# Performance work log

Hardware: AMD Instinct MI355X
Metric: run time of the kernel (lower is better)

## Reference

```python
import jax, jax.numpy as jnp
import numpy as np

HEADS = 4
DIM_HEAD = 32
EPS = 1e-5

def _layernorm(x, g, b):
    mu = jnp.mean(x, axis=-1, keepdims=True)
    var = jnp.var(x, axis=-1, keepdims=True)
    return (x - mu) * jax.lax.rsqrt(var + EPS) * g + b

def setup_inputs() -> dict:
    key = jax.random.key(0)
    ks = jax.random.split(key, 8)
    B, C, H, W = 16, 256, 32, 32
    N = H * W
    inner = HEADS * DIM_HEAD  # 128
    s = lambda d: 1.0 / np.sqrt(d)
    return {
        "x": jax.random.normal(ks[0], (B, C, H, W), jnp.float32),
        "pos_embedding": jax.random.normal(ks[1], (1, N, C), jnp.float32),
        "w_qkv": jax.random.normal(ks[2], (C, inner * 3), jnp.float32) * s(C),
        "w_out": jax.random.normal(ks[3], (inner, C), jnp.float32) * s(inner),
        "b_out": jnp.zeros((C,), jnp.float32),
        "w_ff1": jax.random.normal(ks[4], (C, inner), jnp.float32) * s(C),
        "b_ff1": jnp.zeros((inner,), jnp.float32),
        "w_ff2": jax.random.normal(ks[5], (inner, C), jnp.float32) * s(inner),
        "b_ff2": jnp.zeros((C,), jnp.float32),
        "g1": jnp.ones((C,), jnp.float32),
        "beta1": jnp.zeros((C,), jnp.float32),
        "g2": jnp.ones((C,), jnp.float32),
        "beta2": jnp.zeros((C,), jnp.float32),
    }

def reference(x, pos_embedding, w_qkv, w_out, b_out, w_ff1, b_ff1, w_ff2, b_ff2, g1, beta1, g2, beta2):
    b, c, h, w = x.shape
    n = h * w
    tok = jnp.transpose(x.reshape(b, c, n), (0, 2, 1))  # [b, n, c]
    tok = tok + pos_embedding  # (dropout is identity at eval)
    # attention
    qkv = _layernorm(tok, g1, beta1) @ w_qkv  # [b, n, 3*inner]
    qkv = qkv.reshape(b, n, 3, HEADS, DIM_HEAD)
    q, k, v = qkv[:, :, 0], qkv[:, :, 1], qkv[:, :, 2]  # [b, n, h, d]
    scale = DIM_HEAD ** -0.5
    dots = jnp.einsum('bihd,bjhd->bhij', q, k) * scale
    attn = jax.nn.softmax(dots, axis=-1)
    out = jnp.einsum('bhij,bjhd->bihd', attn, v).reshape(b, n, HEADS * DIM_HEAD)
    tok = out @ w_out + b_out + tok
    # ffn
    hdn = jax.nn.gelu(_layernorm(tok, g2, beta2) @ w_ff1 + b_ff1, approximate=False)
    tok = hdn @ w_ff2 + b_ff2 + tok
    return jnp.transpose(tok, (0, 2, 1)).reshape(b, c, h, w)
```

## Files before the change

### kernel.cpp

```cpp
#include <hip/hip_runtime.h>
#include <hip/hip_bf16.h>
#include <math.h>

#define B_     16
#define C_     256
#define N_     1024
#define HEADS_ 4
#define DH_    32
#define INNER_ 128
#define EPS_   1e-5f

typedef __attribute__((ext_vector_type(8))) short bf16x8;
typedef __attribute__((ext_vector_type(4))) float f32x4;

__device__ __forceinline__ ushort f2bf(float f) {
  union { float f; unsigned u; } v; v.f = f;
  unsigned u = v.u;
  return (ushort)((u + 0x7fffu + ((u >> 16) & 1u)) >> 16);
}
__device__ __forceinline__ float bf2f(ushort u) {
  union { unsigned u; float f; } v; v.u = ((unsigned)u) << 16;
  return v.f;
}
__device__ __forceinline__ unsigned cvt_pk_bf16(float lo, float hi) {
  unsigned r;
  asm("v_cvt_pk_bf16_f32 %0, %1, %2" : "=v"(r) : "v"(lo), "v"(hi));
  return r;
}

#define QSCALE_ 0.2550348652979437f

__global__ __launch_bounds__(256) void k_wconv(
    const float* __restrict__ wqkv, const float* __restrict__ wout,
    const float* __restrict__ wff1, const float* __restrict__ wff2,
    ushort* __restrict__ wqkvT, ushort* __restrict__ woutT,
    ushort* __restrict__ wff1T, ushort* __restrict__ wff2T) {
  int i = blockIdx.x * 256 + threadIdx.x;
  if (i < 98304) {
    int k = i / 384, n = i % 384;
    wqkvT[n * 256 + k] = f2bf(wqkv[i]);
    return;
  }
  i -= 98304;
  if (i < 32768) {
    int k = i / 256, n = i % 256;
    woutT[n * 128 + k] = f2bf(wout[i]);
    return;
  }
  i -= 32768;
  if (i < 32768) {
    int k = i / 128, n = i % 128;
    wff1T[n * 256 + k] = f2bf(wff1[i]);
    return;
  }
  i -= 32768;
  {
    int k = i / 256, n = i % 256;
    wff2T[n * 128 + k] = f2bf(wff2[i]);
  }
}

union KFusedSmem {
  float  xs[C_][68];
  ushort xnl[64][264];
};

__global__ __launch_bounds__(512) void k_fused(
    const float* __restrict__ x, const float* __restrict__ pos,
    const float* __restrict__ g1, const float* __restrict__ beta1,
    const ushort* __restrict__ wqkvT, ushort* __restrict__ tokb,
    ushort* __restrict__ qb, ushort* __restrict__ kb, ushort* __restrict__ vtb) {
  const int b  = blockIdx.x >> 4;
  const int n0 = (blockIdx.x & 15) << 6;
  const int t  = threadIdx.x;
  __shared__ KFusedSmem u;

  {
    const int nq = t & 15, cq = t >> 4;
#pragma unroll
    for (int i = 0; i < 8; ++i) {
      const int c = i * 32 + cq;
      const float4 v = *reinterpret_cast<const float4*>(
          &x[((size_t)b * C_ + c) * N_ + n0 + 4 * nq]);
      *reinterpret_cast<float4*>(&u.xs[c][4 * nq]) = v;
    }
  }
  __syncthreads();

  {
    const int tl = t >> 3, sub = t & 7, c0 = sub * 32;
    const int n = n0 + tl;
    float v[32];
#pragma unroll
    for (int i = 0; i < 32; ++i) v[i] = u.xs[c0 + i][tl];
#pragma unroll
    for (int j = 0; j < 8; ++j) {
      const float4 p = *reinterpret_cast<const float4*>(&pos[(size_t)n * C_ + c0 + 4 * j]);
      v[4*j] += p.x; v[4*j+1] += p.y; v[4*j+2] += p.z; v[4*j+3] += p.w;
    }
    float s = 0.f;
#pragma unroll
    for (int i = 0; i < 32; ++i) s += v[i];
    s += __shfl_xor(s, 1); s += __shfl_xor(s, 2); s += __shfl_xor(s, 4);
    const float mu = s * (1.f / C_);
    float sq = 0.f;
#pragma unroll
    for (int i = 0; i < 32; ++i) { const float d = v[i] - mu; sq += d * d; }
    sq += __shfl_xor(sq, 1); sq += __shfl_xor(sq, 2); sq += __shfl_xor(sq, 4);
    const float rs = rsqrtf(sq * (1.f / C_) + EPS_);

    ushort* tokrow = &tokb[((size_t)b * N_ + n) * C_ + c0];
    ushort xn_local[32];
#pragma unroll
    for (int j = 0; j < 8; ++j) {
      ushort4 tu;
      tu.x = f2bf(v[4*j]);   tu.y = f2bf(v[4*j+1]);
      tu.z = f2bf(v[4*j+2]); tu.w = f2bf(v[4*j+3]);
      *reinterpret_cast<ushort4*>(&tokrow[4 * j]) = tu;
      const float4 g  = *reinterpret_cast<const float4*>(&g1[c0 + 4 * j]);
      const float4 be = *reinterpret_cast<const float4*>(&beta1[c0 + 4 * j]);
      xn_local[4*j]   = f2bf((v[4*j]   - mu) * rs * g.x + be.x);
      xn_local[4*j+1] = f2bf((v[4*j+1] - mu) * rs * g.y + be.y);
      xn_local[4*j+2] = f2bf((v[4*j+2] - mu) * rs * g.z + be.z);
      xn_local[4*j+3] = f2bf((v[4*j+3] - mu) * rs * g.w + be.w);
    }
    __syncthreads();
#pragma unroll
    for (int j = 0; j < 8; ++j)
      *reinterpret_cast<ushort4*>(&u.xnl[tl][c0 + 4 * j]) =
          *reinterpret_cast<ushort4*>(&xn_local[4 * j]);
  }
  __syncthreads();

  {
    const int w = t >> 6, lane = t & 63;
    const int li = lane & 15, g = lane >> 4;
#pragma unroll
    for (int mf = 0; mf < 3; ++mf) {
      const int chb = w * 48 + mf * 16;
      bf16x8 Af[8];
#pragma unroll
      for (int ks = 0; ks < 8; ++ks)
        Af[ks] = *reinterpret_cast<const bf16x8*>(
            &wqkvT[(size_t)(chb + li) * C_ + ks * 32 + 8 * g]);
#pragma unroll
      for (int nf = 0; nf < 4; ++nf) {
        bf16x8 Bf[8];
#pragma unroll
        for (int ks = 0; ks < 8; ++ks)
          Bf[ks] = *reinterpret_cast<const bf16x8*>(&u.xnl[nf * 16 + li][ks * 32 + 8 * g]);
        f32x4 acc = {0.f, 0.f, 0.f, 0.f};
#pragma unroll
        for (int ks = 0; ks < 8; ++ks)
          acc = __builtin_amdgcn_mfma_f32_16x16x32_bf16(Af[ks], Bf[ks], acc, 0, 0, 0);
        const int nn = n0 + nf * 16 + li;
        const int ch0 = chb + 4 * g;
        if (ch0 < 128) {
          const int h = ch0 >> 5, dh = ch0 & 31;
          ushort4 uq;
          uq.x = f2bf(acc[0] * QSCALE_); uq.y = f2bf(acc[1] * QSCALE_);
          uq.z = f2bf(acc[2] * QSCALE_); uq.w = f2bf(acc[3] * QSCALE_);
          *reinterpret_cast<ushort4*>(&qb[(((size_t)(b * HEADS_ + h)) * N_ + nn) * DH_ + dh]) = uq;
        } else if (ch0 < 256) {
          const int c2 = ch0 - 128, h = c2 >> 5, dh = c2 & 31;
          ushort4 uk;
          uk.x = f2bf(acc[0]); uk.y = f2bf(acc[1]); uk.z = f2bf(acc[2]); uk.w = f2bf(acc[3]);
          *reinterpret_cast<ushort4*>(&kb[(((size_t)(b * HEADS_ + h)) * N_ + nn) * DH_ + dh]) = uk;
        } else {
          const int c2 = ch0 - 256, h = c2 >> 5, dh = c2 & 31;
          ushort* base = &vtb[(((size_t)(b * HEADS_ + h)) * DH_ + dh) * N_ + nn];
          base[0] = f2bf(acc[0]); base[N_] = f2bf(acc[1]);
          base[2 * N_] = f2bf(acc[2]); base[3 * N_] = f2bf(acc[3]);
        }
      }
    }
  }
}

__global__ __launch_bounds__(256) void k_attn_mlp(
    const ushort* __restrict__ qb, const ushort* __restrict__ kb,
    const ushort* __restrict__ vtb, const ushort* __restrict__ tokb,
    const ushort* __restrict__ woutT, const float* __restrict__ b_out,
    const ushort* __restrict__ wff1T, const float* __restrict__ b_ff1,
    const ushort* __restrict__ wff2T, const float* __restrict__ b_ff2,
    const float* __restrict__ g2, const float* __restrict__ beta2,
    float* __restrict__ out) {
  const int bid = (blockIdx.x & 7) * 64 + (blockIdx.x >> 3);
  const int b   = bid >> 5;
  const int tt  = bid & 31;
  const int nq0 = tt * 32;
  const int tid = threadIdx.x;
  const int w = tid >> 6, lane = tid & 63;
  const int qi = lane & 15, g = lane >> 4;

  __shared__ __align__(16) union {
    ushort P[4][2][16][72];
    float  t2s[32][260];
  } u1;
  __shared__ __align__(16) ushort xn2[32][264];
  __shared__ __align__(16) union {
    ushort aos[32][136];
    ushort hsb[32][136];
  } u2;

  {
    const int bh = b * HEADS_ + w;
    const ushort* Kb = kb  + (size_t)bh * N_ * DH_;
    const ushort* Vt = vtb + (size_t)bh * DH_ * N_;

    bf16x8 qf[2];
#pragma unroll
    for (int G = 0; G < 2; ++G)
      qf[G] = *reinterpret_cast<const bf16x8*>(
          qb + ((size_t)bh * N_ + nq0 + G * 16 + qi) * DH_ + 8 * g);

    f32x4 acc[2][2];
#pragma unroll
    for (int G = 0; G < 2; ++G)
#pragma unroll
      for (int d = 0; d < 2; ++d)
#pragma unroll
        for (int r = 0; r < 4; ++r) acc[G][d][r] = 0.f;
    float l[2] = {0.f, 0.f};

    bf16x8 kf[4], vf[2][2];
#pragma unroll
    for (int kt = 0; kt < 4; ++kt)
      kf[kt] = *reinterpret_cast<const bf16x8*>(
          Kb + (size_t)(kt * 16 + qi) * DH_ + 8 * g);
#pragma unroll
    for (int c = 0; c < 2; ++c)
#pragma unroll
      for (int d = 0; d < 2; ++d)
        vf[c][d] = *reinterpret_cast<const bf16x8*>(
            Vt + (size_t)(d * 16 + qi) * N_ + c * 32 + 8 * g);

    for (int jt = 0; jt < 16; ++jt) {
      const int kn = (jt < 15 ? jt + 1 : 15) * 64;
      bf16x8 kfn[4], vfn[2][2];
#pragma unroll
      for (int kt = 0; kt < 4; ++kt)
        kfn[kt] = *reinterpret_cast<const bf16x8*>(
            Kb + (size_t)(kn + kt * 16 + qi) * DH_ + 8 * g);
#pragma unroll
      for (int c = 0; c < 2; ++c)
#pragma unroll
        for (int d = 0; d < 2; ++d)
          vfn[c][d] = *reinterpret_cast<const bf16x8*>(
              Vt + (size_t)(d * 16 + qi) * N_ + kn + c * 32 + 8 * g);

      f32x4 s[2][4];
#pragma unroll
      for (int G = 0; G < 2; ++G)
#pragma unroll
        for (int kt = 0; kt < 4; ++kt) {
          f32x4 z = {0.f, 0.f, 0.f, 0.f};
          s[G][kt] = __builtin_amdgcn_mfma_f32_16x16x32_bf16(kf[kt], qf[G], z, 0, 0, 0);
        }

#pragma unroll
      for (int G = 0; G < 2; ++G) {
        float psum = 0.f;
#pragma unroll
        for (int kt = 0; kt < 4; ++kt) {
          const float p0 = exp2f(s[G][kt][0]);
          const float p1 = exp2f(s[G][kt][1]);
          const float p2 = exp2f(s[G][kt][2]);
          const float p3 = exp2f(s[G][kt][3]);
          psum += (p0 + p1) + (p2 + p3);
          uint2 dw;
          dw.x = cvt_pk_bf16(p0, p1);
          dw.y = cvt_pk_bf16(p2, p3);
          *reinterpret_cast<uint2*>(&u1.P[w][G][qi][kt * 16 + 4 * g]) = dw;
        }
        l[G] += psum;
      }

#pragma unroll
      for (int c = 0; c < 2; ++c) {
        const bf16x8 pf0 = *reinterpret_cast<const bf16x8*>(&u1.P[w][0][qi][c * 32 + 8 * g]);
        const bf16x8 pf1 = *reinterpret_cast<const bf16x8*>(&u1.P[w][1][qi][c * 32 + 8 * g]);
#pragma unroll
        for (int d = 0; d < 2; ++d) {
          acc[0][d] = __builtin_amdgcn_mfma_f32_16x16x32_bf16(vf[c][d], pf0, acc[0][d], 0, 0, 0);
          acc[1][d] = __builtin_amdgcn_mfma_f32_16x16x32_bf16(vf[c][d], pf1, acc[1][d], 0, 0, 0);
        }
      }

#pragma unroll
      for (int kt = 0; kt < 4; ++kt) kf[kt] = kfn[kt];
#pragma unroll
      for (int c = 0; c < 2; ++c)
#pragma unroll
        for (int d = 0; d < 2; ++d) vf[c][d] = vfn[c][d];
    }

#pragma unroll
    for (int G = 0; G < 2; ++G) {
      float lg = l[G];
      lg += __shfl_xor(lg, 16);
      lg += __shfl_xor(lg, 32);
      const float inv = 1.f / lg;
      const int nloc = G * 16 + qi;
#pragma unroll
      for (int d = 0; d < 2; ++d) {
        ushort4 uo;
        uo.x = f2bf(acc[G][d][0] * inv);
        uo.y = f2bf(acc[G][d][1] * inv);
        uo.z = f2bf(acc[G][d][2] * inv);
        uo.w = f2bf(acc[G][d][3] * inv);
        *reinterpret_cast<ushort4*>(&u2.aos[nloc][w * 32 + d * 16 + 4 * g]) = uo;
      }
    }
  }
  __syncthreads();

  const int li = qi;

  {
    bf16x8 Af[2][4];
#pragma unroll
    for (int mf = 0; mf < 2; ++mf)
#pragma unroll
      for (int ks = 0; ks < 4; ++ks)
        Af[mf][ks] = *reinterpret_cast<const bf16x8*>(&u2.aos[mf * 16 + li][ks * 32 + 8 * g]);
#pragma unroll
    for (int nf = 0; nf < 4; ++nf) {
      const int n = w * 64 + nf * 16;
      bf16x8 Bf[4];
#pragma unroll
      for (int ks = 0; ks < 4; ++ks)
        Bf[ks] = *reinterpret_cast<const bf16x8*>(
            &woutT[(size_t)(n + li) * INNER_ + ks * 32 + 8 * g]);
#pragma unroll
      for (int mf = 0; mf < 2; ++mf) {
        f32x4 acc = {0.f, 0.f, 0.f, 0.f};
#pragma unroll
        for (int ks = 0; ks < 4; ++ks)
          acc = __builtin_amdgcn_mfma_f32_16x16x32_bf16(Af[mf][ks], Bf[ks], acc, 0, 0, 0);
        const int nch = n + li;
        const int tl0 = mf * 16 + 4 * g;
        const float bo = b_out[nch];
#pragma unroll
        for (int r = 0; r < 4; ++r)
          u1.t2s[tl0 + r][nch] =
              acc[r] + bo + bf2f(tokb[((size_t)b * N_ + nq0 + tl0 + r) * C_ + nch]);
      }
    }
  }
  __syncthreads();

  {
    const int tl = tid >> 3, c0 = (tid & 7) * 32;
    float v[32];
#pragma unroll
    for (int j = 0; j < 8; ++j) {
      const float4 t4 = *reinterpret_cast<const float4*>(&u1.t2s[tl][c0 + 4 * j]);
      v[4*j] = t4.x; v[4*j+1] = t4.y; v[4*j+2] = t4.z; v[4*j+3] = t4.w;
    }
    float s = 0.f;
#pragma unroll
    for (int i = 0; i < 32; ++i) s += v[i];
    s += __shfl_xor(s, 1); s += __shfl_xor(s, 2); s += __shfl_xor(s, 4);
    const float mu = s * (1.f / C_);
    float sq = 0.f;
#pragma unroll
    for (int i = 0; i < 32; ++i) { const float d = v[i] - mu; sq += d * d; }
    sq += __shfl_xor(sq, 1); sq += __shfl_xor(sq, 2); sq += __shfl_xor(sq, 4);
    const float rs = rsqrtf(sq * (1.f / C_) + EPS_);
#pragma unroll
    for (int j = 0; j < 8; ++j) {
      const float4 gg = *reinterpret_cast<const float4*>(&g2[c0 + 4 * j]);
      const float4 be = *reinterpret_cast<const float4*>(&beta2[c0 + 4 * j]);
      ushort4 uu;
      uu.x = f2bf((v[4*j]   - mu) * rs * gg.x + be.x);
      uu.y = f2bf((v[4*j+1] - mu) * rs * gg.y + be.y);
      uu.z = f2bf((v[4*j+2] - mu) * rs * gg.z + be.z);
      uu.w = f2bf((v[4*j+3] - mu) * rs * gg.w + be.w);
      *reinterpret_cast<ushort4*>(&xn2[tl][c0 + 4 * j]) = uu;
    }
  }
  __syncthreads();

  {
    bf16x8 Af[2][8];
#pragma unroll
    for (int mf = 0; mf < 2; ++mf)
#pragma unroll
      for (int ks = 0; ks < 8; ++ks)
        Af[mf][ks] = *reinterpret_cast<const bf16x8*>(&xn2[mf * 16 + li][ks * 32 + 8 * g]);
#pragma unroll
    for (int nf = 0; nf < 2; ++nf) {
      const int n = w * 32 + nf * 16;
      bf16x8 Bf[8];
#pragma unroll
      for (int ks = 0; ks < 8; ++ks)
        Bf[ks] = *reinterpret_cast<const bf16x8*>(
            &wff1T[(size_t)(n + li) * C_ + ks * 32 + 8 * g]);
#pragma unroll
      for (int mf = 0; mf < 2; ++mf) {
        f32x4 acc = {0.f, 0.f, 0.f, 0.f};
#pragma unroll
        for (int ks = 0; ks < 8; ++ks)
          acc = __builtin_amdgcn_mfma_f32_16x16x32_bf16(Af[mf][ks], Bf[ks], acc, 0, 0, 0);
        const int nch = n + li;
        const int tl0 = mf * 16 + 4 * g;
        const float bf1 = b_ff1[nch];
#pragma unroll
        for (int r = 0; r < 4; ++r) {
          float hv = acc[r] + bf1;
          hv = 0.5f * hv * (1.f + erff(hv * 0.70710678118654752f));
          u2.hsb[tl0 + r][nch] = f2bf(hv);
        }
      }
    }
  }
  __syncthreads();

  {
    bf16x8 Af[2][4];
#pragma unroll
    for (int mf = 0; mf < 2; ++mf)
#pragma unroll
      for (int ks = 0; ks < 4; ++ks)
        Af[mf][ks] = *reinterpret_cast<const bf16x8*>(&u2.hsb[mf * 16 + li][ks * 32 + 8 * g]);
#pragma unroll
    for (int nf = 0; nf < 4; ++nf) {
      const int n = w * 64 + nf * 16;
      bf16x8 Bf[4];
#pragma unroll
      for (int ks = 0; ks < 4; ++ks)
        Bf[ks] = *reinterpret_cast<const bf16x8*>(
            &wff2T[(size_t)(n + li) * INNER_ + ks * 32 + 8 * g]);
#pragma unroll
      for (int mf = 0; mf < 2; ++mf) {
        f32x4 acc = {0.f, 0.f, 0.f, 0.f};
#pragma unroll
        for (int ks = 0; ks < 4; ++ks)
          acc = __builtin_amdgcn_mfma_f32_16x16x32_bf16(Af[mf][ks], Bf[ks], acc, 0, 0, 0);
        const int nch = n + li;
        const int tl0 = mf * 16 + 4 * g;
        const float bo = b_ff2[nch];
        float4 o;
        o.x = acc[0] + bo + u1.t2s[tl0 + 0][nch];
        o.y = acc[1] + bo + u1.t2s[tl0 + 1][nch];
        o.z = acc[2] + bo + u1.t2s[tl0 + 2][nch];
        o.w = acc[3] + bo + u1.t2s[tl0 + 3][nch];
        *reinterpret_cast<float4*>(
            &out[((size_t)b * C_ + nch) * N_ + nq0 + tl0]) = o;
      }
    }
  }
}

extern "C" void kernel_launch(void* const* d_in, const int* in_sizes, int n_in,
                              void* d_out, int out_size, void* d_ws, size_t ws_size,
                              hipStream_t stream) {
  const float* x     = (const float*)d_in[0];
  const float* pos   = (const float*)d_in[1];
  const float* w_qkv = (const float*)d_in[2];
  const float* w_out = (const float*)d_in[3];
  const float* b_out = (const float*)d_in[4];
  const float* w_ff1 = (const float*)d_in[5];
  const float* b_ff1 = (const float*)d_in[6];
  const float* w_ff2 = (const float*)d_in[7];
  const float* b_ff2 = (const float*)d_in[8];
  const float* g1    = (const float*)d_in[9];
  const float* beta1 = (const float*)d_in[10];
  const float* g2    = (const float*)d_in[11];
  const float* beta2 = (const float*)d_in[12];
  float* out = (float*)d_out;

  ushort* tokb  = (ushort*)d_ws;
  ushort* qb    = tokb + 4194304;
  ushort* kb    = qb + 2097152;
  ushort* vtb   = kb + 2097152;
  ushort* wqkvT = vtb + 2097152;
  ushort* woutT = wqkvT + 98304;
  ushort* wff1T = woutT + 32768;
  ushort* wff2T = wff1T + 32768;

  k_wconv<<<768, 256, 0, stream>>>(w_qkv, w_out, w_ff1, w_ff2,
                                   wqkvT, woutT, wff1T, wff2T);
  k_fused<<<256, 512, 0, stream>>>(x, pos, g1, beta1, wqkvT, tokb, qb, kb, vtb);
  k_attn_mlp<<<512, 256, 0, stream>>>(qb, kb, vtb, tokb, woutT, b_out,
                                      wff1T, b_ff1, wff2T, b_ff2, g2, beta2, out);
}
```

Baseline: 157.9 us.

## Split attention keys across two wave groups and double block size to 512 threads

Each attention block now runs 8 waves instead of 4. Each head is handled by two waves, and each wave processes half of the key range (8 tiles instead of 16). The partial outputs and row sums are combined through shared memory, with no max correction because the softmax is unnormalized exp2. The MLP phases are redistributed over the 8 waves with narrower per-wave output slices. This doubles the parallelism per block and shortens the serial key loop, at the cost of more shared memory, an extra combine step with barriers, and possible occupancy limits from launch_bounds(512,4).

```diff
diff --git a/kernel.cpp b/kernel.cpp
--- a/kernel.cpp
+++ b/kernel.cpp
@@ -177,7 +177,7 @@
   }
 }
 
-__global__ __launch_bounds__(256) void k_attn_mlp(
+__global__ __launch_bounds__(512, 4) void k_attn_mlp(
     const ushort* __restrict__ qb, const ushort* __restrict__ kb,
     const ushort* __restrict__ vtb, const ushort* __restrict__ tokb,
     const ushort* __restrict__ woutT, const float* __restrict__ b_out,
@@ -191,11 +191,16 @@
   const int nq0 = tt * 32;
   const int tid = threadIdx.x;
   const int w = tid >> 6, lane = tid & 63;
+  const int h = w & 3, kh = w >> 2;
   const int qi = lane & 15, g = lane >> 4;
 
   __shared__ __align__(16) union {
-    ushort P[4][2][16][72];
+    ushort P[8][2][16][72];
     float  t2s[32][260];
+    struct {
+      float O[4][2][2][16][18];
+      float l[4][2][16];
+    } cmb;
   } u1;
   __shared__ __align__(16) ushort xn2[32][264];
   __shared__ __align__(16) union {
@@ -203,8 +208,17 @@
     ushort hsb[32][136];
   } u2;
 
-  {
-    const int bh = b * HEADS_ + w;
+  f32x4 acc[2][2];
+#pragma unroll
+  for (int G = 0; G < 2; ++G)
+#pragma unroll
+    for (int d = 0; d < 2; ++d)
+#pragma unroll
+      for (int r = 0; r < 4; ++r) acc[G][d][r] = 0.f;
+  float lg[2] = {0.f, 0.f};
+
+  {
+    const int bh = b * HEADS_ + h;
     const ushort* Kb = kb  + (size_t)bh * N_ * DH_;
     const ushort* Vt = vtb + (size_t)bh * DH_ * N_;
 
@@ -214,29 +228,24 @@
       qf[G] = *reinterpret_cast<const bf16x8*>(
           qb + ((size_t)bh * N_ + nq0 + G * 16 + qi) * DH_ + 8 * g);
 
-    f32x4 acc[2][2];
-#pragma unroll
-    for (int G = 0; G < 2; ++G)
-#pragma unroll
-      for (int d = 0; d < 2; ++d)
-#pragma unroll
-        for (int r = 0; r < 4; ++r) acc[G][d][r] = 0.f;
-    float l[2] = {0.f, 0.f};
-
+    const int kbase = kh * 8;
     bf16x8 kf[4], vf[2][2];
-#pragma unroll
-    for (int kt = 0; kt < 4; ++kt)
-      kf[kt] = *reinterpret_cast<const bf16x8*>(
-          Kb + (size_t)(kt * 16 + qi) * DH_ + 8 * g);
-#pragma unroll
-    for (int c = 0; c < 2; ++c)
-#pragma unroll
-      for (int d = 0; d < 2; ++d)
-        vf[c][d] = *reinterpret_cast<const bf16x8*>(
-            Vt + (size_t)(d * 16 + qi) * N_ + c * 32 + 8 * g);
-
-    for (int jt = 0; jt < 16; ++jt) {
-      const int kn = (jt < 15 ? jt + 1 : 15) * 64;
+    {
+      const int k0 = kbase * 64;
+#pragma unroll
+      for (int kt = 0; kt < 4; ++kt)
+        kf[kt] = *reinterpret_cast<const bf16x8*>(
+            Kb + (size_t)(k0 + kt * 16 + qi) * DH_ + 8 * g);
+#pragma unroll
+      for (int c = 0; c < 2; ++c)
+#pragma unroll
+        for (int d = 0; d < 2; ++d)
+          vf[c][d] = *reinterpret_cast<const bf16x8*>(
+              Vt + (size_t)(d * 16 + qi) * N_ + k0 + c * 32 + 8 * g);
+    }
+
+    for (int jt = 0; jt < 8; ++jt) {
+      const int kn = (kbase + (jt < 7 ? jt + 1 : 7)) * 64;
       bf16x8 kfn[4], vfn[2][2];
 #pragma unroll
       for (int kt = 0; kt < 4; ++kt)
@@ -273,7 +282,7 @@
           dw.y = cvt_pk_bf16(p2, p3);
           *reinterpret_cast<uint2*>(&u1.P[w][G][qi][kt * 16 + 4 * g]) = dw;
         }
-        l[G] += psum;
+        lg[G] += psum;
       }
 
 #pragma unroll
@@ -297,19 +306,40 @@
 
 #pragma unroll
     for (int G = 0; G < 2; ++G) {
-      float lg = l[G];
-      lg += __shfl_xor(lg, 16);
-      lg += __shfl_xor(lg, 32);
-      const float inv = 1.f / lg;
+      lg[G] += __shfl_xor(lg[G], 16);
+      lg[G] += __shfl_xor(lg[G], 32);
+    }
+  }
+
+  __syncthreads();
+
+  if (kh == 1) {
+#pragma unroll
+    for (int G = 0; G < 2; ++G) {
+#pragma unroll
+      for (int d = 0; d < 2; ++d)
+#pragma unroll
+        for (int r = 0; r < 4; ++r)
+          u1.cmb.O[h][G][d][4 * g + r][qi] = acc[G][d][r];
+      if (lane < 16) u1.cmb.l[h][G][qi] = lg[G];
+    }
+  }
+  __syncthreads();
+
+  if (kh == 0) {
+#pragma unroll
+    for (int G = 0; G < 2; ++G) {
+      const float lt = lg[G] + u1.cmb.l[h][G][qi];
+      const float inv = 1.f / lt;
       const int nloc = G * 16 + qi;
 #pragma unroll
       for (int d = 0; d < 2; ++d) {
         ushort4 uo;
-        uo.x = f2bf(acc[G][d][0] * inv);
-        uo.y = f2bf(acc[G][d][1] * inv);
-        uo.z = f2bf(acc[G][d][2] * inv);
-        uo.w = f2bf(acc[G][d][3] * inv);
-        *reinterpret_cast<ushort4*>(&u2.aos[nloc][w * 32 + d * 16 + 4 * g]) = uo;
+        uo.x = f2bf((acc[G][d][0] + u1.cmb.O[h][G][d][4 * g + 0][qi]) * inv);
+        uo.y = f2bf((acc[G][d][1] + u1.cmb.O[h][G][d][4 * g + 1][qi]) * inv);
+        uo.z = f2bf((acc[G][d][2] + u1.cmb.O[h][G][d][4 * g + 2][qi]) * inv);
+        uo.w = f2bf((acc[G][d][3] + u1.cmb.O[h][G][d][4 * g + 3][qi]) * inv);
+        *reinterpret_cast<ushort4*>(&u2.aos[nloc][h * 32 + d * 16 + 4 * g]) = uo;
       }
     }
   }
@@ -325,8 +355,8 @@
       for (int ks = 0; ks < 4; ++ks)
         Af[mf][ks] = *reinterpret_cast<const bf16x8*>(&u2.aos[mf * 16 + li][ks * 32 + 8 * g]);
 #pragma unroll
-    for (int nf = 0; nf < 4; ++nf) {
-      const int n = w * 64 + nf * 16;
+    for (int nf = 0; nf < 2; ++nf) {
+      const int n = w * 32 + nf * 16;
       bf16x8 Bf[4];
 #pragma unroll
       for (int ks = 0; ks < 4; ++ks)
@@ -334,42 +364,44 @@
             &woutT[(size_t)(n + li) * INNER_ + ks * 32 + 8 * g]);
 #pragma unroll
       for (int mf = 0; mf < 2; ++mf) {
-        f32x4 acc = {0.f, 0.f, 0.f, 0.f};
+        f32x4 acc2 = {0.f, 0.f, 0.f, 0.f};
 #pragma unroll
         for (int ks = 0; ks < 4; ++ks)
-          acc = __builtin_amdgcn_mfma_f32_16x16x32_bf16(Af[mf][ks], Bf[ks], acc, 0, 0, 0);
+          acc2 = __builtin_amdgcn_mfma_f32_16x16x32_bf16(Af[mf][ks], Bf[ks], acc2, 0, 0, 0);
         const int nch = n + li;
         const int tl0 = mf * 16 + 4 * g;
         const float bo = b_out[nch];
 #pragma unroll
         for (int r = 0; r < 4; ++r)
           u1.t2s[tl0 + r][nch] =
-              acc[r] + bo + bf2f(tokb[((size_t)b * N_ + nq0 + tl0 + r) * C_ + nch]);
-      }
-    }
-  }
-  __syncthreads();
-
-  {
-    const int tl = tid >> 3, c0 = (tid & 7) * 32;
-    float v[32];
-#pragma unroll
-    for (int j = 0; j < 8; ++j) {
+              acc2[r] + bo + bf2f(tokb[((size_t)b * N_ + nq0 + tl0 + r) * C_ + nch]);
+      }
+    }
+  }
+  __syncthreads();
+
+  {
+    const int tl = tid >> 4, c0 = (tid & 15) * 16;
+    float v[16];
+#pragma unroll
+    for (int j = 0; j < 4; ++j) {
       const float4 t4 = *reinterpret_cast<const float4*>(&u1.t2s[tl][c0 + 4 * j]);
       v[4*j] = t4.x; v[4*j+1] = t4.y; v[4*j+2] = t4.z; v[4*j+3] = t4.w;
     }
     float s = 0.f;
 #pragma unroll
-    for (int i = 0; i < 32; ++i) s += v[i];
-    s += __shfl_xor(s, 1); s += __shfl_xor(s, 2); s += __shfl_xor(s, 4);
+    for (int i = 0; i < 16; ++i) s += v[i];
+    s += __shfl_xor(s, 1); s += __shfl_xor(s, 2);
+    s += __shfl_xor(s, 4); s += __shfl_xor(s, 8);
     const float mu = s * (1.f / C_);
     float sq = 0.f;
 #pragma unroll
-    for (int i = 0; i < 32; ++i) { const float d = v[i] - mu; sq += d * d; }
-    sq += __shfl_xor(sq, 1); sq += __shfl_xor(sq, 2); sq += __shfl_xor(sq, 4);
+    for (int i = 0; i < 16; ++i) { const float d = v[i] - mu; sq += d * d; }
+    sq += __shfl_xor(sq, 1); sq += __shfl_xor(sq, 2);
+    sq += __shfl_xor(sq, 4); sq += __shfl_xor(sq, 8);
     const float rs = rsqrtf(sq * (1.f / C_) + EPS_);
 #pragma unroll
-    for (int j = 0; j < 8; ++j) {
+    for (int j = 0; j < 4; ++j) {
       const float4 gg = *reinterpret_cast<const float4*>(&g2[c0 + 4 * j]);
       const float4 be = *reinterpret_cast<const float4*>(&beta2[c0 + 4 * j]);
       ushort4 uu;
@@ -389,44 +421,41 @@
 #pragma unroll
       for (int ks = 0; ks < 8; ++ks)
         Af[mf][ks] = *reinterpret_cast<const bf16x8*>(&xn2[mf * 16 + li][ks * 32 + 8 * g]);
+    const int n = w * 16;
+    bf16x8 Bf[8];
+#pragma unroll
+    for (int ks = 0; ks < 8; ++ks)
+      Bf[ks] = *reinterpret_cast<const bf16x8*>(
+          &wff1T[(size_t)(n + li) * C_ + ks * 32 + 8 * g]);
+#pragma unroll
+    for (int mf = 0; mf < 2; ++mf) {
+      f32x4 acc2 = {0.f, 0.f, 0.f, 0.f};
+#pragma unroll
+      for (int ks = 0; ks < 8; ++ks)
+        acc2 = __builtin_amdgcn_mfma_f32_16x16x32_bf16(Af[mf][ks], Bf[ks], acc2, 0, 0, 0);
+      const int nch = n + li;
+      const int tl0 = mf * 16 + 4 * g;
+      const float bf1 = b_ff1[nch];
+#pragma unroll
+      for (int r = 0; r < 4; ++r) {
+        float hv = acc2[r] + bf1;
+        hv = 0.5f * hv * (1.f + erff(hv * 0.70710678118654752f));
+        u2.hsb[tl0 + r][nch] = f2bf(hv);
+      }
+    }
+  }
+  __syncthreads();
+
+  {
+    bf16x8 Af[2][4];
+#pragma unroll
+    for (int mf = 0; mf < 2; ++mf)
+#pragma unroll
+      for (int ks = 0; ks < 4; ++ks)
+        Af[mf][ks] = *reinterpret_cast<const bf16x8*>(&u2.hsb[mf * 16 + li][ks * 32 + 8 * g]);
 #pragma unroll
     for (int nf = 0; nf < 2; ++nf) {
       const int n = w * 32 + nf * 16;
-      bf16x8 Bf[8];
-#pragma unroll
-      for (int ks = 0; ks < 8; ++ks)
-        Bf[ks] = *reinterpret_cast<const bf16x8*>(
-            &wff1T[(size_t)(n + li) * C_ + ks * 32 + 8 * g]);
-#pragma unroll
-      for (int mf = 0; mf < 2; ++mf) {
-        f32x4 acc = {0.f, 0.f, 0.f, 0.f};
-#pragma unroll
-        for (int ks = 0; ks < 8; ++ks)
-          acc = __builtin_amdgcn_mfma_f32_16x16x32_bf16(Af[mf][ks], Bf[ks], acc, 0, 0, 0);
-        const int nch = n + li;
-        const int tl0 = mf * 16 + 4 * g;
-        const float bf1 = b_ff1[nch];
-#pragma unroll
-        for (int r = 0; r < 4; ++r) {
-          float hv = acc[r] + bf1;
-          hv = 0.5f * hv * (1.f + erff(hv * 0.70710678118654752f));
-          u2.hsb[tl0 + r][nch] = f2bf(hv);
-        }
-      }
-    }
-  }
-  __syncthreads();
-
-  {
-    bf16x8 Af[2][4];
-#pragma unroll
-    for (int mf = 0; mf < 2; ++mf)
-#pragma unroll
-      for (int ks = 0; ks < 4; ++ks)
-        Af[mf][ks] = *reinterpret_cast<const bf16x8*>(&u2.hsb[mf * 16 + li][ks * 32 + 8 * g]);
-#pragma unroll
-    for (int nf = 0; nf < 4; ++nf) {
-      const int n = w * 64 + nf * 16;
       bf16x8 Bf[4];
 #pragma unroll
       for (int ks = 0; ks < 4; ++ks)
@@ -434,18 +463,18 @@
             &wff2T[(size_t)(n + li) * INNER_ + ks * 32 + 8 * g]);
 #pragma unroll
       for (int mf = 0; mf < 2; ++mf) {
-        f32x4 acc = {0.f, 0.f, 0.f, 0.f};
+        f32x4 acc2 = {0.f, 0.f, 0.f, 0.f};
 #pragma unroll
         for (int ks = 0; ks < 4; ++ks)
-          acc = __builtin_amdgcn_mfma_f32_16x16x32_bf16(Af[mf][ks], Bf[ks], acc, 0, 0, 0);
+          acc2 = __builtin_amdgcn_mfma_f32_16x16x32_bf16(Af[mf][ks], Bf[ks], acc2, 0, 0, 0);
         const int nch = n + li;
         const int tl0 = mf * 16 + 4 * g;
         const float bo = b_ff2[nch];
         float4 o;
-        o.x = acc[0] + bo + u1.t2s[tl0 + 0][nch];
-        o.y = acc[1] + bo + u1.t2s[tl0 + 1][nch];
-        o.z = acc[2] + bo + u1.t2s[tl0 + 2][nch];
-        o.w = acc[3] + bo + u1.t2s[tl0 + 3][nch];
+        o.x = acc2[0] + bo + u1.t2s[tl0 + 0][nch];
+        o.y = acc2[1] + bo + u1.t2s[tl0 + 1][nch];
+        o.z = acc2[2] + bo + u1.t2s[tl0 + 2][nch];
+        o.w = acc2[3] + bo + u1.t2s[tl0 + 3][nch];
         *reinterpret_cast<float4*>(
             &out[((size_t)b * C_ + nch) * N_ + nq0 + tl0]) = o;
       }
@@ -483,6 +512,6 @@
   k_wconv<<<768, 256, 0, stream>>>(w_qkv, w_out, w_ff1, w_ff2,
                                    wqkvT, woutT, wff1T, wff2T);
   k_fused<<<256, 512, 0, stream>>>(x, pos, g1, beta1, wqkvT, tokb, qb, kb, vtb);
-  k_attn_mlp<<<512, 256, 0, stream>>>(qb, kb, vtb, tokb, woutT, b_out,
+  k_attn_mlp<<<512, 512, 0, stream>>>(qb, kb, vtb, tokb, woutT, b_out,
                                       wff1T, b_ff1, wff2T, b_ff2, g2, beta2, out);
 }
```

Result: no change. 158.9 us (+0.6%).
